# Optimization experiments

Measured on AMD Instinct MI355X. Metric: run time of the kernel, lower is better.

Reference implementation:

```python
import jax, jax.numpy as jnp
import numpy as np

B, S, D = 2, 2048, 1024
N_HEAD, D_ATTN = 16, 64


def setup_inputs() -> dict:
    key = jax.random.key(0)
    ks = jax.random.split(key, 5)
    x = jax.random.normal(ks[0], (B, S, D), dtype=jnp.float32)
    # causal mask: True = masked (as consumed by torch.masked_fill)
    mask = jnp.triu(jnp.ones((S, S), dtype=bool), k=1)
    scale = 0.02
    w_q = jax.random.normal(ks[1], (D, N_HEAD * D_ATTN), dtype=jnp.float32) * scale
    w_k = jax.random.normal(ks[2], (D, N_HEAD * D_ATTN), dtype=jnp.float32) * scale
    w_v = jax.random.normal(ks[3], (D, N_HEAD * D_ATTN), dtype=jnp.float32) * scale
    w_o = jax.random.normal(ks[4], (N_HEAD * D_ATTN, D), dtype=jnp.float32) * scale
    return {"x": x, "mask": mask, "w_q": w_q, "w_k": w_k, "w_v": w_v, "w_o": w_o}


def _split(t):
    # [B,S,H*Da] -> [B,H,S,Da]
    b, s, _ = t.shape
    return t.reshape(b, s, N_HEAD, D_ATTN).transpose(0, 2, 1, 3)


def reference(x, mask, w_q, w_k, w_v, w_o):
    q = _split(x @ w_q)
    k = _split(x @ w_k)
    v = _split(x @ w_v)
    scale = D_ATTN ** 0.5
    score = jnp.einsum("bhqd,bhkd->bhqk", q, k) / scale  # [B,H,S,S]
    score = jnp.where(mask, -jnp.inf, score)
    prob = jax.nn.softmax(score, axis=-1)
    out = jnp.einsum("bhqk,bhkd->bhqd", prob, v)
    out = out.transpose(0, 2, 1, 3).reshape(x.shape[0], x.shape[1], N_HEAD * D_ATTN)
    return out @ w_o
```

## Files before the change

kernel.cpp:

```cpp
#include <hip/hip_runtime.h>
#include <stdint.h>

using u16 = unsigned short;
using u32 = unsigned int;
using u64 = unsigned long long;

typedef float f32x4 __attribute__((ext_vector_type(4)));
typedef __bf16 bf16x8 __attribute__((ext_vector_type(8)));

#define DEV static __device__ __forceinline__

DEV u16 f2bf(float f) {
  u32 u = __float_as_uint(f);
  u += 0x7FFFu + ((u >> 16) & 1u);
  return (u16)(u >> 16);
}

DEV void gld16(const void* g, void* l) {
  __builtin_amdgcn_global_load_lds((__attribute__((address_space(1))) void*)g,
                                   (__attribute__((address_space(3))) void*)l,
                                   16, 0, 0);
}

__global__ void k_cvt_x(const float* __restrict__ x, u16* __restrict__ xb) {
  int i = (blockIdx.x * 256 + threadIdx.x) * 8;
  float4 a = *(const float4*)&x[i];
  float4 b = *(const float4*)&x[i + 4];
  __align__(16) u16 o[8];
  o[0] = f2bf(a.x); o[1] = f2bf(a.y); o[2] = f2bf(a.z); o[3] = f2bf(a.w);
  o[4] = f2bf(b.x); o[5] = f2bf(b.y); o[6] = f2bf(b.z); o[7] = f2bf(b.w);
  *(uint4*)&xb[i] = *(const uint4*)o;
}

__global__ void k_cvt_w(const float* __restrict__ w0, const float* __restrict__ w1,
                        const float* __restrict__ w2, const float* __restrict__ w3,
                        u16* __restrict__ t0, u16* __restrict__ t1,
                        u16* __restrict__ t2, u16* __restrict__ t3) {
  const float* w = blockIdx.z == 0 ? w0 : blockIdx.z == 1 ? w1 : blockIdx.z == 2 ? w2 : w3;
  u16* wt       = blockIdx.z == 0 ? t0 : blockIdx.z == 1 ? t1 : blockIdx.z == 2 ? t2 : t3;
  __shared__ __align__(16) float tile[64][68];
  const int tid = threadIdx.x;
  const int k0 = blockIdx.x * 64, n0 = blockIdx.y * 64;
#pragma unroll
  for (int i = 0; i < 4; ++i) {
    int c = tid + i * 256;
    int kr = c >> 4, col = (c & 15) * 4;
    *(float4*)&tile[kr][col] = *(const float4*)&w[(size_t)(k0 + kr) * 1024 + n0 + col];
  }
  __syncthreads();
#pragma unroll
  for (int i = 0; i < 2; ++i) {
    int c = tid + i * 256;
    int nr = c >> 3, kc = (c & 7) * 8;
    __align__(16) u16 o[8];
#pragma unroll
    for (int j = 0; j < 8; ++j) o[j] = f2bf(tile[kc + j][nr]);
    *(uint4*)&wt[(size_t)(n0 + nr) * 1024 + k0 + kc] = *(const uint4*)o;
  }
}

DEV void gemm_mainloop(const u16* __restrict__ A, const u16* __restrict__ Bt,
                       int m0, int n0, u16* Asb, u16* Bsb, f32x4 (&acc)[4][4]) {
  const int tid = threadIdx.x;
  const int lane = tid & 63;
  const int wv = tid >> 6;
  const int wm = (wv >> 1) * 64, wn = (wv & 1) * 64;

#pragma unroll
  for (int i = 0; i < 4; ++i)
#pragma unroll
    for (int j = 0; j < 4; ++j) {
      f32x4 z = {0.f, 0.f, 0.f, 0.f};
      acc[i][j] = z;
    }

  const int c0 = wv * 64 + lane, c1 = c0 + 256;
  const int r0 = c0 >> 2, r1 = c1 >> 2;
  const int b0 = (c0 & 3) ^ (r0 & 3) ^ ((r0 >> 2) & 3);
  const int b1 = (c1 & 3) ^ (r1 & 3) ^ ((r1 >> 2) & 3);
  const u16* ga0 = A + (size_t)(m0 + r0) * 1024 + b0 * 8;
  const u16* ga1 = A + (size_t)(m0 + r1) * 1024 + b1 * 8;
  const u16* gb0 = Bt + (size_t)(n0 + r0) * 1024 + b0 * 8;
  const u16* gb1 = Bt + (size_t)(n0 + r1) * 1024 + b1 * 8;
  u16* la0 = Asb + (wv * 64) * 8;
  u16* la1 = Asb + (wv * 64 + 256) * 8;
  u16* lb0 = Bsb + (wv * 64) * 8;
  u16* lb1 = Bsb + (wv * 64 + 256) * 8;

  int aoff[4], boff[4];
#pragma unroll
  for (int f = 0; f < 4; ++f) {
    int ra = wm + f * 16 + (lane & 15);
    aoff[f] = ra * 32 + (((lane >> 4) ^ (ra & 3) ^ ((ra >> 2) & 3)) * 8);
    int rb = wn + f * 16 + (lane & 15);
    boff[f] = rb * 32 + (((lane >> 4) ^ (rb & 3) ^ ((rb >> 2) & 3)) * 8);
  }

  for (int kt = 0; kt < 32; ++kt) {
    const int k0 = kt * 32;
    gld16(ga0 + k0, la0);
    gld16(ga1 + k0, la1);
    gld16(gb0 + k0, lb0);
    gld16(gb1 + k0, lb1);
    __syncthreads();
    bf16x8 af[4], bfv[4];
#pragma unroll
    for (int f = 0; f < 4; ++f) af[f] = *(const bf16x8*)&Asb[aoff[f]];
#pragma unroll
    for (int f = 0; f < 4; ++f) bfv[f] = *(const bf16x8*)&Bsb[boff[f]];
#pragma unroll
    for (int i = 0; i < 4; ++i)
#pragma unroll
      for (int j = 0; j < 4; ++j)
        acc[i][j] = __builtin_amdgcn_mfma_f32_16x16x32_bf16(af[i], bfv[j], acc[i][j], 0, 0, 0);
    __syncthreads();
  }
}

__global__ __launch_bounds__(256) void k_gemm_qkv(
    const u16* __restrict__ X, const u16* __restrict__ Wq, const u16* __restrict__ Wk,
    const u16* __restrict__ Wv, u16* __restrict__ Q, u16* __restrict__ K,
    u16* __restrict__ V) {
  __shared__ __align__(16) u16 Asb[128 * 32];
  __shared__ __align__(16) u16 Bsb[128 * 32];
  const int nb = blockIdx.x, mb = blockIdx.y;
  const int proj = nb >> 3, n0 = (nb & 7) * 128;
  const u16* W = proj == 0 ? Wq : proj == 1 ? Wk : Wv;
  u16* Dst = proj == 0 ? Q : proj == 1 ? K : V;
  const float scl = proj == 0 ? 0.125f * 1.4426950408889634f : 1.0f;
  f32x4 acc[4][4];
  gemm_mainloop(X, W, mb * 128, n0, Asb, Bsb, acc);
  const int lane = threadIdx.x & 63, wv = threadIdx.x >> 6;
  const int wm = (wv >> 1) * 64, wn = (wv & 1) * 64;
#pragma unroll
  for (int i = 0; i < 4; ++i)
#pragma unroll
    for (int j = 0; j < 4; ++j)
#pragma unroll
      for (int r = 0; r < 4; ++r) {
        int m = mb * 128 + wm + i * 16 + (lane >> 4) * 4 + r;
        int n = n0 + wn + j * 16 + (lane & 15);
        int b = m >> 11, s = m & 2047, h = n >> 6, d = n & 63;
        Dst[(size_t)((b * 16 + h) * 2048 + s) * 64 + d] = f2bf(acc[i][j][r] * scl);
      }
}

__global__ __launch_bounds__(256) void k_gemm_out(
    const u16* __restrict__ A, const u16* __restrict__ Wt, float* __restrict__ Out) {
  __shared__ __align__(16) u16 Asb[128 * 32];
  __shared__ __align__(16) u16 Bsb[128 * 32];
  const int nb = blockIdx.x, mb = blockIdx.y;
  f32x4 acc[4][4];
  gemm_mainloop(A, Wt, mb * 128, nb * 128, Asb, Bsb, acc);
  const int lane = threadIdx.x & 63, wv = threadIdx.x >> 6;
  const int wm = (wv >> 1) * 64, wn = (wv & 1) * 64;
#pragma unroll
  for (int i = 0; i < 4; ++i)
#pragma unroll
    for (int j = 0; j < 4; ++j)
#pragma unroll
      for (int r = 0; r < 4; ++r) {
        int m = mb * 128 + wm + i * 16 + (lane >> 4) * 4 + r;
        int n = nb * 128 + wn + j * 16 + (lane & 15);
        Out[(size_t)m * 1024 + n] = acc[i][j][r];
      }
}

__global__ void k_transpose_v(const u16* __restrict__ V, u16* __restrict__ Vt) {
  __shared__ __align__(16) u16 t[64][80];
  const int bh = blockIdx.y, s0 = blockIdx.x * 64;
  const int tid = threadIdx.x;
#pragma unroll
  for (int i = 0; i < 2; ++i) {
    int c = tid + i * 256;
    int sr = c >> 3, dc = (c & 7) * 8;
    *(uint4*)&t[sr][dc] = *(const uint4*)&V[((size_t)bh * 2048 + s0 + sr) * 64 + dc];
  }
  __syncthreads();
#pragma unroll
  for (int i = 0; i < 2; ++i) {
    int c = tid + i * 256;
    int dr = c >> 3, c7 = c & 7;
    __align__(8) u16 o[8];
#pragma unroll
    for (int j = 0; j < 8; ++j) o[j] = t[c7 * 8 + j][dr];
    int bp = ((c7 >> 1) & 1) * 32 + (c7 & 1) * 16 + ((c7 >> 2) & 1) * 4;
    u16* row = &Vt[((size_t)bh * 64 + dr) * 2048 + s0];
    *(u64*)&row[bp]     = *(const u64*)&o[0];
    *(u64*)&row[bp + 8] = *(const u64*)&o[4];
  }
}

__global__ __launch_bounds__(256) void k_attn(
    const u16* __restrict__ Qg, const u16* __restrict__ Kg,
    const u16* __restrict__ Vtg, u16* __restrict__ Og) {
  __shared__ __align__(16) u16 Ks[2][64 * 64];
  __shared__ __align__(16) u16 Vs[2][64 * 64];
  const int tid = threadIdx.x, lane = tid & 63, wv = tid >> 6;
  const int lo = lane & 15, hi = lane >> 4;
  const int jpair = blockIdx.x, bh = blockIdx.y;
  const u16* Qb = Qg + (size_t)bh * 2048 * 64;
  const u16* Kb = Kg + (size_t)bh * 2048 * 64;
  const u16* Vb = Vtg + (size_t)bh * 64 * 2048;
  const int b = bh >> 4, h = bh & 15;

  const int c0 = wv * 64 + lane, c1 = c0 + 256;
  const int r0 = c0 >> 3, r1 = c1 >> 3;
  const int e0 = ((c0 & 7) ^ (r0 & 7)) * 8;
  const int e1 = ((c1 & 7) ^ (r1 & 7)) * 8;

#pragma unroll 1
  for (int pass = 0; pass < 2; ++pass) {
    const int qt = pass == 0 ? jpair : 31 - jpair;
    const int q0 = qt * 64;
    const int nt = qt + 1;
    const int qq = q0 + wv * 16 + lo;

    bf16x8 qf[2];
#pragma unroll
    for (int kf = 0; kf < 2; ++kf)
      qf[kf] = *(const bf16x8*)&Qb[(size_t)(q0 + wv * 16 + lo) * 64 + kf * 32 + hi * 8];

    f32x4 ao[4];
#pragma unroll
    for (int df = 0; df < 4; ++df) {
      f32x4 z = {0.f, 0.f, 0.f, 0.f};
      ao[df] = z;
    }
    float m_run = -1e30f, l_run = 0.f;

    gld16(Kb + (size_t)r0 * 64 + e0, &Ks[0][wv * 512]);
    gld16(Kb + (size_t)r1 * 64 + e1, &Ks[0][wv * 512 + 2048]);
    gld16(Vb + (size_t)r0 * 2048 + e0, &Vs[0][wv * 512]);
    gld16(Vb + (size_t)r1 * 2048 + e1, &Vs[0][wv * 512 + 2048]);
    __syncthreads();

    int cur = 0;
#pragma unroll 1
    for (int t = 0; t < nt; ++t) {
      const int kv0 = t * 64;
      if (t + 1 < nt) {
        const int kn = kv0 + 64;
        gld16(Kb + (size_t)(kn + r0) * 64 + e0, &Ks[cur ^ 1][wv * 512]);
        gld16(Kb + (size_t)(kn + r1) * 64 + e1, &Ks[cur ^ 1][wv * 512 + 2048]);
        gld16(Vb + (size_t)r0 * 2048 + kn + e0, &Vs[cur ^ 1][wv * 512]);
        gld16(Vb + (size_t)r1 * 2048 + kn + e1, &Vs[cur ^ 1][wv * 512 + 2048]);
      }

      f32x4 sc[4];
#pragma unroll
      for (int cf = 0; cf < 4; ++cf) {
        f32x4 z = {0.f, 0.f, 0.f, 0.f};
        sc[cf] = z;
#pragma unroll
        for (int kf = 0; kf < 2; ++kf) {
          int row = cf * 16 + lo;
          int blk = ((kf * 4 + hi) ^ (row & 7)) * 8;
          bf16x8 kfr = *(const bf16x8*)&Ks[cur][row * 64 + blk];
          sc[cf] = __builtin_amdgcn_mfma_f32_16x16x32_bf16(kfr, qf[kf], sc[cf], 0, 0, 0);
        }
      }

      if (t == nt - 1) {
#pragma unroll
        for (int cf = 0; cf < 4; ++cf)
#pragma unroll
          for (int r = 0; r < 4; ++r) {
            int kk = kv0 + cf * 16 + hi * 4 + r;
            if (kk > qq) sc[cf][r] = -1e30f;
          }
      }

      float mx0 = fmaxf(fmaxf(sc[0][0], sc[0][1]), fmaxf(sc[0][2], sc[0][3]));
      float mx1 = fmaxf(fmaxf(sc[1][0], sc[1][1]), fmaxf(sc[1][2], sc[1][3]));
      float mx2 = fmaxf(fmaxf(sc[2][0], sc[2][1]), fmaxf(sc[2][2], sc[2][3]));
      float mx3 = fmaxf(fmaxf(sc[3][0], sc[3][1]), fmaxf(sc[3][2], sc[3][3]));
      float mx = fmaxf(fmaxf(mx0, mx1), fmaxf(mx2, mx3));
      mx = fmaxf(mx, __shfl_xor(mx, 16));
      mx = fmaxf(mx, __shfl_xor(mx, 32));

      if (__any(mx > m_run + 8.0f)) {
        float mnew = fmaxf(m_run, mx);
        float sclf = __builtin_amdgcn_exp2f(m_run - mnew);
        const int base = lane & 48;
#pragma unroll
        for (int r = 0; r < 4; ++r) {
          float s_r = __shfl(sclf, base + hi * 4 + r);
#pragma unroll
          for (int df = 0; df < 4; ++df) ao[df][r] *= s_r;
        }
        l_run *= sclf;
        m_run = mnew;
      }

      float pp[4];
      bf16x8 pa0, pa1;
#pragma unroll
      for (int cf = 0; cf < 4; ++cf) {
        float p0 = __builtin_amdgcn_exp2f(sc[cf][0] - m_run);
        float p1 = __builtin_amdgcn_exp2f(sc[cf][1] - m_run);
        float p2 = __builtin_amdgcn_exp2f(sc[cf][2] - m_run);
        float p3 = __builtin_amdgcn_exp2f(sc[cf][3] - m_run);
        pp[cf] = (p0 + p1) + (p2 + p3);
        bf16x8& pa = (cf & 1) ? pa1 : pa0;
        int j = (cf >> 1) * 4;
        pa[j] = (__bf16)p0; pa[j + 1] = (__bf16)p1;
        pa[j + 2] = (__bf16)p2; pa[j + 3] = (__bf16)p3;
      }
      float psum = (pp[0] + pp[1]) + (pp[2] + pp[3]);
      psum += __shfl_xor(psum, 16);
      psum += __shfl_xor(psum, 32);
      l_run += psum;

#pragma unroll
      for (int df = 0; df < 4; ++df) {
#pragma unroll
        for (int kf = 0; kf < 2; ++kf) {
          int row = df * 16 + lo;
          int blk = ((kf * 4 + hi) ^ (row & 7)) * 8;
          bf16x8 vfr = *(const bf16x8*)&Vs[cur][row * 64 + blk];
          ao[df] = __builtin_amdgcn_mfma_f32_16x16x32_bf16(kf == 0 ? pa0 : pa1, vfr,
                                                           ao[df], 0, 0, 0);
        }
      }
      __syncthreads();
      cur ^= 1;
    }

    float linv[4];
    const int base = lane & 48;
#pragma unroll
    for (int r = 0; r < 4; ++r) {
      float l_r = __shfl(l_run, base + hi * 4 + r);
      linv[r] = 1.0f / l_r;
    }
#pragma unroll
    for (int df = 0; df < 4; ++df)
#pragma unroll
      for (int r = 0; r < 4; ++r) {
        int s = q0 + wv * 16 + hi * 4 + r;
        int d = df * 16 + lo;
        Og[((size_t)(b * 2048 + s)) * 1024 + h * 64 + d] = f2bf(ao[df][r] * linv[r]);
      }
    __syncthreads();
  }
}

extern "C" void kernel_launch(void* const* d_in, const int* in_sizes, int n_in,
                              void* d_out, int out_size, void* d_ws, size_t ws_size,
                              hipStream_t stream) {
  const float* x = (const float*)d_in[0];
  const float* wq = (const float*)d_in[2];
  const float* wk = (const float*)d_in[3];
  const float* wv = (const float*)d_in[4];
  const float* wo = (const float*)d_in[5];

  char* ws = (char*)d_ws;
  u16* xb  = (u16*)(ws);
  u16* wqt = (u16*)(ws + 8388608);
  u16* wkt = (u16*)(ws + 8388608 + 2097152);
  u16* wvt = (u16*)(ws + 8388608 + 2 * 2097152);
  u16* wot = (u16*)(ws + 8388608 + 3 * 2097152);
  u16* qb  = (u16*)(ws + 16777216);
  u16* kb  = (u16*)(ws + 16777216 + 8388608);
  u16* vb  = (u16*)(ws + 16777216 + 2 * 8388608);
  u16* vt  = (u16*)(ws + 16777216 + 3 * 8388608);
  u16* ao  = (u16*)(ws + 16777216 + 4 * 8388608);

  k_cvt_x<<<dim3(2048), dim3(256), 0, stream>>>(x, xb);
  k_cvt_w<<<dim3(16, 16, 4), dim3(256), 0, stream>>>(wq, wk, wv, wo, wqt, wkt, wvt, wot);
  k_gemm_qkv<<<dim3(24, 32), dim3(256), 0, stream>>>(xb, wqt, wkt, wvt, qb, kb, vb);
  k_transpose_v<<<dim3(32, 32), dim3(256), 0, stream>>>(vb, vt);
  k_attn<<<dim3(16, 32), dim3(256), 0, stream>>>(qb, kb, vt, ao);
  k_gemm_out<<<dim3(8, 32), dim3(256), 0, stream>>>(ao, wot, (float*)d_out);
}
```

Measured before the change: 128.8 us.

## Double-buffer GEMM LDS tiles and fuse paired attention query tiles into one KV sweep

The GEMM mainloop now double-buffers its LDS tiles and prefetches the next K slice while computing the current one, which removes one barrier per iteration. The attention kernel processes both causal query tiles of a pair in a single sweep over K/V, so the shared prefix tiles are loaded once instead of twice. It also adds s_setprio around the MFMA sections and remaps blocks to XCDs so that the heads sharing K/V land together. The cost is doubled LDS in the GEMMs and higher register pressure from two sets of accumulators in attention.

```diff
diff --git a/kernel.cpp b/kernel.cpp
--- a/kernel.cpp
+++ b/kernel.cpp
@@ -82,10 +82,7 @@
   const u16* ga1 = A + (size_t)(m0 + r1) * 1024 + b1 * 8;
   const u16* gb0 = Bt + (size_t)(n0 + r0) * 1024 + b0 * 8;
   const u16* gb1 = Bt + (size_t)(n0 + r1) * 1024 + b1 * 8;
-  u16* la0 = Asb + (wv * 64) * 8;
-  u16* la1 = Asb + (wv * 64 + 256) * 8;
-  u16* lb0 = Bsb + (wv * 64) * 8;
-  u16* lb1 = Bsb + (wv * 64 + 256) * 8;
+  const int da0 = (wv * 64) * 8, da1 = (wv * 64 + 256) * 8;
 
   int aoff[4], boff[4];
 #pragma unroll
@@ -96,18 +93,27 @@
     boff[f] = rb * 32 + (((lane >> 4) ^ (rb & 3) ^ ((rb >> 2) & 3)) * 8);
   }
 
+  gld16(ga0, Asb + da0);
+  gld16(ga1, Asb + da1);
+  gld16(gb0, Bsb + da0);
+  gld16(gb1, Bsb + da1);
+  __syncthreads();
+
   for (int kt = 0; kt < 32; ++kt) {
-    const int k0 = kt * 32;
-    gld16(ga0 + k0, la0);
-    gld16(ga1 + k0, la1);
-    gld16(gb0 + k0, lb0);
-    gld16(gb1 + k0, lb1);
-    __syncthreads();
+    const int cur = (kt & 1) * 4096;
+    if (kt + 1 < 32) {
+      const int nxt = 4096 - cur;
+      const int k0 = (kt + 1) * 32;
+      gld16(ga0 + k0, Asb + nxt + da0);
+      gld16(ga1 + k0, Asb + nxt + da1);
+      gld16(gb0 + k0, Bsb + nxt + da0);
+      gld16(gb1 + k0, Bsb + nxt + da1);
+    }
     bf16x8 af[4], bfv[4];
 #pragma unroll
-    for (int f = 0; f < 4; ++f) af[f] = *(const bf16x8*)&Asb[aoff[f]];
-#pragma unroll
-    for (int f = 0; f < 4; ++f) bfv[f] = *(const bf16x8*)&Bsb[boff[f]];
+    for (int f = 0; f < 4; ++f) af[f] = *(const bf16x8*)&Asb[cur + aoff[f]];
+#pragma unroll
+    for (int f = 0; f < 4; ++f) bfv[f] = *(const bf16x8*)&Bsb[cur + boff[f]];
 #pragma unroll
     for (int i = 0; i < 4; ++i)
 #pragma unroll
@@ -121,8 +127,8 @@
     const u16* __restrict__ X, const u16* __restrict__ Wq, const u16* __restrict__ Wk,
     const u16* __restrict__ Wv, u16* __restrict__ Q, u16* __restrict__ K,
     u16* __restrict__ V) {
-  __shared__ __align__(16) u16 Asb[128 * 32];
-  __shared__ __align__(16) u16 Bsb[128 * 32];
+  __shared__ __align__(16) u16 Asb[2 * 128 * 32];
+  __shared__ __align__(16) u16 Bsb[2 * 128 * 32];
   const int nb = blockIdx.x, mb = blockIdx.y;
   const int proj = nb >> 3, n0 = (nb & 7) * 128;
   const u16* W = proj == 0 ? Wq : proj == 1 ? Wk : Wv;
@@ -147,8 +153,8 @@
 
 __global__ __launch_bounds__(256) void k_gemm_out(
     const u16* __restrict__ A, const u16* __restrict__ Wt, float* __restrict__ Out) {
-  __shared__ __align__(16) u16 Asb[128 * 32];
-  __shared__ __align__(16) u16 Bsb[128 * 32];
+  __shared__ __align__(16) u16 Asb[2 * 128 * 32];
+  __shared__ __align__(16) u16 Bsb[2 * 128 * 32];
   const int nb = blockIdx.x, mb = blockIdx.y;
   f32x4 acc[4][4];
   gemm_mainloop(A, Wt, mb * 128, nb * 128, Asb, Bsb, acc);
@@ -189,6 +195,79 @@
     *(u64*)&row[bp]     = *(const u64*)&o[0];
     *(u64*)&row[bp + 8] = *(const u64*)&o[4];
   }
+}
+
+DEV void qk_tile(const u16* Kc, const bf16x8 (&qf)[2], int lo, int hi, f32x4 (&sc)[4]) {
+#pragma unroll
+  for (int cf = 0; cf < 4; ++cf) {
+    f32x4 z = {0.f, 0.f, 0.f, 0.f};
+    sc[cf] = z;
+#pragma unroll
+    for (int kf = 0; kf < 2; ++kf) {
+      int row = cf * 16 + lo;
+      int blk = ((kf * 4 + hi) ^ (row & 7)) * 8;
+      bf16x8 kfr = *(const bf16x8*)&Kc[row * 64 + blk];
+      sc[cf] = __builtin_amdgcn_mfma_f32_16x16x32_bf16(kfr, qf[kf], sc[cf], 0, 0, 0);
+    }
+  }
+}
+
+DEV void sm_pv(f32x4 (&sc)[4], const u16* Vc, int lane, int lo, int hi,
+               float& m_run, float& l_run, f32x4 (&ao)[4]) {
+  float mx0 = fmaxf(fmaxf(sc[0][0], sc[0][1]), fmaxf(sc[0][2], sc[0][3]));
+  float mx1 = fmaxf(fmaxf(sc[1][0], sc[1][1]), fmaxf(sc[1][2], sc[1][3]));
+  float mx2 = fmaxf(fmaxf(sc[2][0], sc[2][1]), fmaxf(sc[2][2], sc[2][3]));
+  float mx3 = fmaxf(fmaxf(sc[3][0], sc[3][1]), fmaxf(sc[3][2], sc[3][3]));
+  float mx = fmaxf(fmaxf(mx0, mx1), fmaxf(mx2, mx3));
+  mx = fmaxf(mx, __shfl_xor(mx, 16));
+  mx = fmaxf(mx, __shfl_xor(mx, 32));
+
+  if (__any(mx > m_run + 8.0f)) {
+    float mnew = fmaxf(m_run, mx);
+    float sclf = __builtin_amdgcn_exp2f(m_run - mnew);
+    const int base = lane & 48;
+#pragma unroll
+    for (int r = 0; r < 4; ++r) {
+      float s_r = __shfl(sclf, base + hi * 4 + r);
+#pragma unroll
+      for (int df = 0; df < 4; ++df) ao[df][r] *= s_r;
+    }
+    l_run *= sclf;
+    m_run = mnew;
+  }
+
+  float pp[4];
+  bf16x8 pa0, pa1;
+#pragma unroll
+  for (int cf = 0; cf < 4; ++cf) {
+    float p0 = __builtin_amdgcn_exp2f(sc[cf][0] - m_run);
+    float p1 = __builtin_amdgcn_exp2f(sc[cf][1] - m_run);
+    float p2 = __builtin_amdgcn_exp2f(sc[cf][2] - m_run);
+    float p3 = __builtin_amdgcn_exp2f(sc[cf][3] - m_run);
+    pp[cf] = (p0 + p1) + (p2 + p3);
+    bf16x8& pa = (cf & 1) ? pa1 : pa0;
+    int j = (cf >> 1) * 4;
+    pa[j] = (__bf16)p0; pa[j + 1] = (__bf16)p1;
+    pa[j + 2] = (__bf16)p2; pa[j + 3] = (__bf16)p3;
+  }
+  float psum = (pp[0] + pp[1]) + (pp[2] + pp[3]);
+  psum += __shfl_xor(psum, 16);
+  psum += __shfl_xor(psum, 32);
+  l_run += psum;
+
+  __builtin_amdgcn_s_setprio(1);
+#pragma unroll
+  for (int df = 0; df < 4; ++df) {
+#pragma unroll
+    for (int kf = 0; kf < 2; ++kf) {
+      int row = df * 16 + lo;
+      int blk = ((kf * 4 + hi) ^ (row & 7)) * 8;
+      bf16x8 vfr = *(const bf16x8*)&Vc[row * 64 + blk];
+      ao[df] = __builtin_amdgcn_mfma_f32_16x16x32_bf16(kf == 0 ? pa0 : pa1, vfr,
+                                                       ao[df], 0, 0, 0);
+    }
+  }
+  __builtin_amdgcn_s_setprio(0);
 }
 
 __global__ __launch_bounds__(256) void k_attn(
@@ -198,137 +277,103 @@
   __shared__ __align__(16) u16 Vs[2][64 * 64];
   const int tid = threadIdx.x, lane = tid & 63, wv = tid >> 6;
   const int lo = lane & 15, hi = lane >> 4;
-  const int jpair = blockIdx.x, bh = blockIdx.y;
+
+  const int flat = blockIdx.y * 16 + blockIdx.x;
+  const int xcd = flat & 7, slot = flat >> 3;
+  const int bh = xcd * 4 + (slot >> 4);
+  const int jpair = slot & 15;
+
   const u16* Qb = Qg + (size_t)bh * 2048 * 64;
   const u16* Kb = Kg + (size_t)bh * 2048 * 64;
   const u16* Vb = Vtg + (size_t)bh * 64 * 2048;
   const int b = bh >> 4, h = bh & 15;
 
+  const int q0A = jpair * 64, q0B = (31 - jpair) * 64;
+  const int nta = jpair + 1, ntb = 32 - jpair;
+  const int qqA = q0A + wv * 16 + lo, qqB = q0B + wv * 16 + lo;
+
+  bf16x8 qfA[2], qfB[2];
+#pragma unroll
+  for (int kf = 0; kf < 2; ++kf) {
+    qfA[kf] = *(const bf16x8*)&Qb[(size_t)(q0A + wv * 16 + lo) * 64 + kf * 32 + hi * 8];
+    qfB[kf] = *(const bf16x8*)&Qb[(size_t)(q0B + wv * 16 + lo) * 64 + kf * 32 + hi * 8];
+  }
+
+  f32x4 aoA[4], aoB[4];
+#pragma unroll
+  for (int df = 0; df < 4; ++df) {
+    f32x4 z = {0.f, 0.f, 0.f, 0.f};
+    aoA[df] = z;
+    aoB[df] = z;
+  }
+  float mA = -1e30f, lA = 0.f, mB = -1e30f, lB = 0.f;
+
   const int c0 = wv * 64 + lane, c1 = c0 + 256;
   const int r0 = c0 >> 3, r1 = c1 >> 3;
   const int e0 = ((c0 & 7) ^ (r0 & 7)) * 8;
   const int e1 = ((c1 & 7) ^ (r1 & 7)) * 8;
 
+  gld16(Kb + (size_t)r0 * 64 + e0, &Ks[0][wv * 512]);
+  gld16(Kb + (size_t)r1 * 64 + e1, &Ks[0][wv * 512 + 2048]);
+  gld16(Vb + (size_t)r0 * 2048 + e0, &Vs[0][wv * 512]);
+  gld16(Vb + (size_t)r1 * 2048 + e1, &Vs[0][wv * 512 + 2048]);
+  __syncthreads();
+
 #pragma unroll 1
+  for (int t = 0; t < ntb; ++t) {
+    const u16* Kc = Ks[t & 1];
+    const u16* Vc = Vs[t & 1];
+    if (t + 1 < ntb) {
+      const int kn = (t + 1) * 64;
+      u16* kd = Ks[(t + 1) & 1];
+      u16* vd = Vs[(t + 1) & 1];
+      gld16(Kb + (size_t)(kn + r0) * 64 + e0, kd + wv * 512);
+      gld16(Kb + (size_t)(kn + r1) * 64 + e1, kd + wv * 512 + 2048);
+      gld16(Vb + (size_t)r0 * 2048 + kn + e0, vd + wv * 512);
+      gld16(Vb + (size_t)r1 * 2048 + kn + e1, vd + wv * 512 + 2048);
+    }
+    const bool doA = (t < nta);
+
+    f32x4 scB[4], scA[4];
+    __builtin_amdgcn_s_setprio(1);
+    qk_tile(Kc, qfB, lo, hi, scB);
+    if (doA) qk_tile(Kc, qfA, lo, hi, scA);
+    __builtin_amdgcn_s_setprio(0);
+
+    if (t == ntb - 1) {
+      const int kv0 = t * 64;
+#pragma unroll
+      for (int cf = 0; cf < 4; ++cf)
+#pragma unroll
+        for (int r = 0; r < 4; ++r) {
+          int kk = kv0 + cf * 16 + hi * 4 + r;
+          if (kk > qqB) scB[cf][r] = -1e30f;
+        }
+    }
+    if (doA && t == nta - 1) {
+      const int kv0 = t * 64;
+#pragma unroll
+      for (int cf = 0; cf < 4; ++cf)
+#pragma unroll
+        for (int r = 0; r < 4; ++r) {
+          int kk = kv0 + cf * 16 + hi * 4 + r;
+          if (kk > qqA) scA[cf][r] = -1e30f;
+        }
+    }
+
+    sm_pv(scB, Vc, lane, lo, hi, mB, lB, aoB);
+    if (doA) sm_pv(scA, Vc, lane, lo, hi, mA, lA, aoA);
+
+    __syncthreads();
+  }
+
+  const int base = lane & 48;
+#pragma unroll
   for (int pass = 0; pass < 2; ++pass) {
-    const int qt = pass == 0 ? jpair : 31 - jpair;
-    const int q0 = qt * 64;
-    const int nt = qt + 1;
-    const int qq = q0 + wv * 16 + lo;
-
-    bf16x8 qf[2];
-#pragma unroll
-    for (int kf = 0; kf < 2; ++kf)
-      qf[kf] = *(const bf16x8*)&Qb[(size_t)(q0 + wv * 16 + lo) * 64 + kf * 32 + hi * 8];
-
-    f32x4 ao[4];
-#pragma unroll
-    for (int df = 0; df < 4; ++df) {
-      f32x4 z = {0.f, 0.f, 0.f, 0.f};
-      ao[df] = z;
-    }
-    float m_run = -1e30f, l_run = 0.f;
-
-    gld16(Kb + (size_t)r0 * 64 + e0, &Ks[0][wv * 512]);
-    gld16(Kb + (size_t)r1 * 64 + e1, &Ks[0][wv * 512 + 2048]);
-    gld16(Vb + (size_t)r0 * 2048 + e0, &Vs[0][wv * 512]);
-    gld16(Vb + (size_t)r1 * 2048 + e1, &Vs[0][wv * 512 + 2048]);
-    __syncthreads();
-
-    int cur = 0;
-#pragma unroll 1
-    for (int t = 0; t < nt; ++t) {
-      const int kv0 = t * 64;
-      if (t + 1 < nt) {
-        const int kn = kv0 + 64;
-        gld16(Kb + (size_t)(kn + r0) * 64 + e0, &Ks[cur ^ 1][wv * 512]);
-        gld16(Kb + (size_t)(kn + r1) * 64 + e1, &Ks[cur ^ 1][wv * 512 + 2048]);
-        gld16(Vb + (size_t)r0 * 2048 + kn + e0, &Vs[cur ^ 1][wv * 512]);
-        gld16(Vb + (size_t)r1 * 2048 + kn + e1, &Vs[cur ^ 1][wv * 512 + 2048]);
-      }
-
-      f32x4 sc[4];
-#pragma unroll
-      for (int cf = 0; cf < 4; ++cf) {
-        f32x4 z = {0.f, 0.f, 0.f, 0.f};
-        sc[cf] = z;
-#pragma unroll
-        for (int kf = 0; kf < 2; ++kf) {
-          int row = cf * 16 + lo;
-          int blk = ((kf * 4 + hi) ^ (row & 7)) * 8;
-          bf16x8 kfr = *(const bf16x8*)&Ks[cur][row * 64 + blk];
-          sc[cf] = __builtin_amdgcn_mfma_f32_16x16x32_bf16(kfr, qf[kf], sc[cf], 0, 0, 0);
-        }
-      }
-
-      if (t == nt - 1) {
-#pragma unroll
-        for (int cf = 0; cf < 4; ++cf)
-#pragma unroll
-          for (int r = 0; r < 4; ++r) {
-            int kk = kv0 + cf * 16 + hi * 4 + r;
-            if (kk > qq) sc[cf][r] = -1e30f;
-          }
-      }
-
-      float mx0 = fmaxf(fmaxf(sc[0][0], sc[0][1]), fmaxf(sc[0][2], sc[0][3]));
-      float mx1 = fmaxf(fmaxf(sc[1][0], sc[1][1]), fmaxf(sc[1][2], sc[1][3]));
-      float mx2 = fmaxf(fmaxf(sc[2][0], sc[2][1]), fmaxf(sc[2][2], sc[2][3]));
-      float mx3 = fmaxf(fmaxf(sc[3][0], sc[3][1]), fmaxf(sc[3][2], sc[3][3]));
-      float mx = fmaxf(fmaxf(mx0, mx1), fmaxf(mx2, mx3));
-      mx = fmaxf(mx, __shfl_xor(mx, 16));
-      mx = fmaxf(mx, __shfl_xor(mx, 32));
-
-      if (__any(mx > m_run + 8.0f)) {
-        float mnew = fmaxf(m_run, mx);
-        float sclf = __builtin_amdgcn_exp2f(m_run - mnew);
-        const int base = lane & 48;
-#pragma unroll
-        for (int r = 0; r < 4; ++r) {
-          float s_r = __shfl(sclf, base + hi * 4 + r);
-#pragma unroll
-          for (int df = 0; df < 4; ++df) ao[df][r] *= s_r;
-        }
-        l_run *= sclf;
-        m_run = mnew;
-      }
-
-      float pp[4];
-      bf16x8 pa0, pa1;
-#pragma unroll
-      for (int cf = 0; cf < 4; ++cf) {
-        float p0 = __builtin_amdgcn_exp2f(sc[cf][0] - m_run);
-        float p1 = __builtin_amdgcn_exp2f(sc[cf][1] - m_run);
-        float p2 = __builtin_amdgcn_exp2f(sc[cf][2] - m_run);
-        float p3 = __builtin_amdgcn_exp2f(sc[cf][3] - m_run);
-        pp[cf] = (p0 + p1) + (p2 + p3);
-        bf16x8& pa = (cf & 1) ? pa1 : pa0;
-        int j = (cf >> 1) * 4;
-        pa[j] = (__bf16)p0; pa[j + 1] = (__bf16)p1;
-        pa[j + 2] = (__bf16)p2; pa[j + 3] = (__bf16)p3;
-      }
-      float psum = (pp[0] + pp[1]) + (pp[2] + pp[3]);
-      psum += __shfl_xor(psum, 16);
-      psum += __shfl_xor(psum, 32);
-      l_run += psum;
-
-#pragma unroll
-      for (int df = 0; df < 4; ++df) {
-#pragma unroll
-        for (int kf = 0; kf < 2; ++kf) {
-          int row = df * 16 + lo;
-          int blk = ((kf * 4 + hi) ^ (row & 7)) * 8;
-          bf16x8 vfr = *(const bf16x8*)&Vs[cur][row * 64 + blk];
-          ao[df] = __builtin_amdgcn_mfma_f32_16x16x32_bf16(kf == 0 ? pa0 : pa1, vfr,
-                                                           ao[df], 0, 0, 0);
-        }
-      }
-      __syncthreads();
-      cur ^= 1;
-    }
-
+    const f32x4* ao = pass == 0 ? aoA : aoB;
+    const float l_run = pass == 0 ? lA : lB;
+    const int q0 = pass == 0 ? q0A : q0B;
     float linv[4];
-    const int base = lane & 48;
 #pragma unroll
     for (int r = 0; r < 4; ++r) {
       float l_r = __shfl(l_run, base + hi * 4 + r);
@@ -342,7 +387,6 @@
         int d = df * 16 + lo;
         Og[((size_t)(b * 2048 + s)) * 1024 + h * 64 + d] = f2bf(ao[df][r] * linv[r]);
       }
-    __syncthreads();
   }
 }
 
```

After: 132.6 us. 2.9% more time.

## Fuse V transpose into QKV GEMM epilogue and remap attention grid per XCD

Applied to the files above, without the earlier changes.

The QKV GEMM now writes V directly in the transposed, permuted layout that attention consumes, which removes the separate transpose kernel and its round trip through global memory. The attention kernel drops the paired-pass scheme and launches one block per query tile, longest tiles first, with block indices remapped so the heads are grouped by XCD for L2 locality. MFMA phases are wrapped in s_setprio so matrix work gets scheduling priority. The risks are uncoalesced 8-byte scattered stores in the GEMM epilogue and load imbalance from one-tile blocks.

```diff
diff --git a/kernel.cpp b/kernel.cpp
--- a/kernel.cpp
+++ b/kernel.cpp
@@ -120,29 +120,49 @@
 __global__ __launch_bounds__(256) void k_gemm_qkv(
     const u16* __restrict__ X, const u16* __restrict__ Wq, const u16* __restrict__ Wk,
     const u16* __restrict__ Wv, u16* __restrict__ Q, u16* __restrict__ K,
-    u16* __restrict__ V) {
+    u16* __restrict__ Vt) {
   __shared__ __align__(16) u16 Asb[128 * 32];
   __shared__ __align__(16) u16 Bsb[128 * 32];
   const int nb = blockIdx.x, mb = blockIdx.y;
   const int proj = nb >> 3, n0 = (nb & 7) * 128;
   const u16* W = proj == 0 ? Wq : proj == 1 ? Wk : Wv;
-  u16* Dst = proj == 0 ? Q : proj == 1 ? K : V;
   const float scl = proj == 0 ? 0.125f * 1.4426950408889634f : 1.0f;
   f32x4 acc[4][4];
   gemm_mainloop(X, W, mb * 128, n0, Asb, Bsb, acc);
   const int lane = threadIdx.x & 63, wv = threadIdx.x >> 6;
+  const int lo = lane & 15, hi = lane >> 4;
   const int wm = (wv >> 1) * 64, wn = (wv & 1) * 64;
-#pragma unroll
-  for (int i = 0; i < 4; ++i)
-#pragma unroll
-    for (int j = 0; j < 4; ++j)
-#pragma unroll
-      for (int r = 0; r < 4; ++r) {
-        int m = mb * 128 + wm + i * 16 + (lane >> 4) * 4 + r;
-        int n = n0 + wn + j * 16 + (lane & 15);
-        int b = m >> 11, s = m & 2047, h = n >> 6, d = n & 63;
-        Dst[(size_t)((b * 16 + h) * 2048 + s) * 64 + d] = f2bf(acc[i][j][r] * scl);
+
+  if (proj == 2) {
+    const int stile = mb * 128 + wm;
+    const int b = stile >> 11, sb = stile & 2047;
+#pragma unroll
+    for (int i = 0; i < 4; ++i) {
+      const int kp = (i & 1) * 32 + (hi >> 1) * 16 + (hi & 1) * 8 + (i >> 1) * 4;
+#pragma unroll
+      for (int j = 0; j < 4; ++j) {
+        int n = n0 + wn + j * 16 + lo;
+        int h = n >> 6, d = n & 63;
+        __align__(8) u16 o[4];
+#pragma unroll
+        for (int r = 0; r < 4; ++r) o[r] = f2bf(acc[i][j][r]);
+        *(u64*)&Vt[((size_t)((b * 16 + h) * 64 + d)) * 2048 + sb + kp] = *(const u64*)o;
       }
+    }
+  } else {
+    u16* Dst = proj == 0 ? Q : K;
+#pragma unroll
+    for (int i = 0; i < 4; ++i)
+#pragma unroll
+      for (int j = 0; j < 4; ++j)
+#pragma unroll
+        for (int r = 0; r < 4; ++r) {
+          int m = mb * 128 + wm + i * 16 + hi * 4 + r;
+          int n = n0 + wn + j * 16 + lo;
+          int b = m >> 11, s = m & 2047, h = n >> 6, d = n & 63;
+          Dst[(size_t)((b * 16 + h) * 2048 + s) * 64 + d] = f2bf(acc[i][j][r] * scl);
+        }
+  }
 }
 
 __global__ __launch_bounds__(256) void k_gemm_out(
@@ -166,29 +186,77 @@
       }
 }
 
-__global__ void k_transpose_v(const u16* __restrict__ V, u16* __restrict__ Vt) {
-  __shared__ __align__(16) u16 t[64][80];
-  const int bh = blockIdx.y, s0 = blockIdx.x * 64;
-  const int tid = threadIdx.x;
-#pragma unroll
-  for (int i = 0; i < 2; ++i) {
-    int c = tid + i * 256;
-    int sr = c >> 3, dc = (c & 7) * 8;
-    *(uint4*)&t[sr][dc] = *(const uint4*)&V[((size_t)bh * 2048 + s0 + sr) * 64 + dc];
-  }
-  __syncthreads();
-#pragma unroll
-  for (int i = 0; i < 2; ++i) {
-    int c = tid + i * 256;
-    int dr = c >> 3, c7 = c & 7;
-    __align__(8) u16 o[8];
-#pragma unroll
-    for (int j = 0; j < 8; ++j) o[j] = t[c7 * 8 + j][dr];
-    int bp = ((c7 >> 1) & 1) * 32 + (c7 & 1) * 16 + ((c7 >> 2) & 1) * 4;
-    u16* row = &Vt[((size_t)bh * 64 + dr) * 2048 + s0];
-    *(u64*)&row[bp]     = *(const u64*)&o[0];
-    *(u64*)&row[bp + 8] = *(const u64*)&o[4];
-  }
+DEV void qk_tile(const u16* Kc, const bf16x8 (&qf)[2], int lo, int hi, f32x4 (&sc)[4]) {
+#pragma unroll
+  for (int cf = 0; cf < 4; ++cf) {
+    f32x4 z = {0.f, 0.f, 0.f, 0.f};
+    sc[cf] = z;
+#pragma unroll
+    for (int kf = 0; kf < 2; ++kf) {
+      int row = cf * 16 + lo;
+      int blk = ((kf * 4 + hi) ^ (row & 7)) * 8;
+      bf16x8 kfr = *(const bf16x8*)&Kc[row * 64 + blk];
+      sc[cf] = __builtin_amdgcn_mfma_f32_16x16x32_bf16(kfr, qf[kf], sc[cf], 0, 0, 0);
+    }
+  }
+}
+
+DEV void sm_pv(f32x4 (&sc)[4], const u16* Vc, int lane, int lo, int hi,
+               float& m_run, float& l_run, f32x4 (&ao)[4]) {
+  float mx0 = fmaxf(fmaxf(sc[0][0], sc[0][1]), fmaxf(sc[0][2], sc[0][3]));
+  float mx1 = fmaxf(fmaxf(sc[1][0], sc[1][1]), fmaxf(sc[1][2], sc[1][3]));
+  float mx2 = fmaxf(fmaxf(sc[2][0], sc[2][1]), fmaxf(sc[2][2], sc[2][3]));
+  float mx3 = fmaxf(fmaxf(sc[3][0], sc[3][1]), fmaxf(sc[3][2], sc[3][3]));
+  float mx = fmaxf(fmaxf(mx0, mx1), fmaxf(mx2, mx3));
+  mx = fmaxf(mx, __shfl_xor(mx, 16));
+  mx = fmaxf(mx, __shfl_xor(mx, 32));
+
+  if (__any(mx > m_run + 8.0f)) {
+    float mnew = fmaxf(m_run, mx);
+    float sclf = __builtin_amdgcn_exp2f(m_run - mnew);
+    const int base = lane & 48;
+#pragma unroll
+    for (int r = 0; r < 4; ++r) {
+      float s_r = __shfl(sclf, base + hi * 4 + r);
+#pragma unroll
+      for (int df = 0; df < 4; ++df) ao[df][r] *= s_r;
+    }
+    l_run *= sclf;
+    m_run = mnew;
+  }
+
+  float pp[4];
+  bf16x8 pa0, pa1;
+#pragma unroll
+  for (int cf = 0; cf < 4; ++cf) {
+    float p0 = __builtin_amdgcn_exp2f(sc[cf][0] - m_run);
+    float p1 = __builtin_amdgcn_exp2f(sc[cf][1] - m_run);
+    float p2 = __builtin_amdgcn_exp2f(sc[cf][2] - m_run);
+    float p3 = __builtin_amdgcn_exp2f(sc[cf][3] - m_run);
+    pp[cf] = (p0 + p1) + (p2 + p3);
+    bf16x8& pa = (cf & 1) ? pa1 : pa0;
+    int j = (cf >> 1) * 4;
+    pa[j] = (__bf16)p0; pa[j + 1] = (__bf16)p1;
+    pa[j + 2] = (__bf16)p2; pa[j + 3] = (__bf16)p3;
+  }
+  float psum = (pp[0] + pp[1]) + (pp[2] + pp[3]);
+  psum += __shfl_xor(psum, 16);
+  psum += __shfl_xor(psum, 32);
+  l_run += psum;
+
+  __builtin_amdgcn_s_setprio(1);
+#pragma unroll
+  for (int df = 0; df < 4; ++df) {
+#pragma unroll
+    for (int kf = 0; kf < 2; ++kf) {
+      int row = df * 16 + lo;
+      int blk = ((kf * 4 + hi) ^ (row & 7)) * 8;
+      bf16x8 vfr = *(const bf16x8*)&Vc[row * 64 + blk];
+      ao[df] = __builtin_amdgcn_mfma_f32_16x16x32_bf16(kf == 0 ? pa0 : pa1, vfr,
+                                                       ao[df], 0, 0, 0);
+    }
+  }
+  __builtin_amdgcn_s_setprio(0);
 }
 
 __global__ __launch_bounds__(256) void k_attn(
@@ -198,152 +266,95 @@
   __shared__ __align__(16) u16 Vs[2][64 * 64];
   const int tid = threadIdx.x, lane = tid & 63, wv = tid >> 6;
   const int lo = lane & 15, hi = lane >> 4;
-  const int jpair = blockIdx.x, bh = blockIdx.y;
+
+  const int flat = blockIdx.y * 32 + blockIdx.x;
+  const int xcd = flat & 7, slot = flat >> 3;
+  const int bh = xcd * 4 + (slot >> 5);
+  const int qt = 31 - (slot & 31);
+
   const u16* Qb = Qg + (size_t)bh * 2048 * 64;
   const u16* Kb = Kg + (size_t)bh * 2048 * 64;
   const u16* Vb = Vtg + (size_t)bh * 64 * 2048;
   const int b = bh >> 4, h = bh & 15;
 
+  const int q0 = qt * 64;
+  const int nt = qt + 1;
+  const int qq = q0 + wv * 16 + lo;
+
+  bf16x8 qf[2];
+#pragma unroll
+  for (int kf = 0; kf < 2; ++kf)
+    qf[kf] = *(const bf16x8*)&Qb[(size_t)(q0 + wv * 16 + lo) * 64 + kf * 32 + hi * 8];
+
+  f32x4 ao[4];
+#pragma unroll
+  for (int df = 0; df < 4; ++df) {
+    f32x4 z = {0.f, 0.f, 0.f, 0.f};
+    ao[df] = z;
+  }
+  float m_run = -1e30f, l_run = 0.f;
+
   const int c0 = wv * 64 + lane, c1 = c0 + 256;
   const int r0 = c0 >> 3, r1 = c1 >> 3;
   const int e0 = ((c0 & 7) ^ (r0 & 7)) * 8;
   const int e1 = ((c1 & 7) ^ (r1 & 7)) * 8;
 
+  gld16(Kb + (size_t)r0 * 64 + e0, &Ks[0][wv * 512]);
+  gld16(Kb + (size_t)r1 * 64 + e1, &Ks[0][wv * 512 + 2048]);
+  gld16(Vb + (size_t)r0 * 2048 + e0, &Vs[0][wv * 512]);
+  gld16(Vb + (size_t)r1 * 2048 + e1, &Vs[0][wv * 512 + 2048]);
+  __syncthreads();
+
 #pragma unroll 1
-  for (int pass = 0; pass < 2; ++pass) {
-    const int qt = pass == 0 ? jpair : 31 - jpair;
-    const int q0 = qt * 64;
-    const int nt = qt + 1;
-    const int qq = q0 + wv * 16 + lo;
-
-    bf16x8 qf[2];
-#pragma unroll
-    for (int kf = 0; kf < 2; ++kf)
-      qf[kf] = *(const bf16x8*)&Qb[(size_t)(q0 + wv * 16 + lo) * 64 + kf * 32 + hi * 8];
-
-    f32x4 ao[4];
-#pragma unroll
-    for (int df = 0; df < 4; ++df) {
-      f32x4 z = {0.f, 0.f, 0.f, 0.f};
-      ao[df] = z;
-    }
-    float m_run = -1e30f, l_run = 0.f;
-
-    gld16(Kb + (size_t)r0 * 64 + e0, &Ks[0][wv * 512]);
-    gld16(Kb + (size_t)r1 * 64 + e1, &Ks[0][wv * 512 + 2048]);
-    gld16(Vb + (size_t)r0 * 2048 + e0, &Vs[0][wv * 512]);
-    gld16(Vb + (size_t)r1 * 2048 + e1, &Vs[0][wv * 512 + 2048]);
+  for (int t = 0; t < nt; ++t) {
+    const u16* Kc = Ks[t & 1];
+    const u16* Vc = Vs[t & 1];
+    if (t + 1 < nt) {
+      const int kn = (t + 1) * 64;
+      u16* kd = Ks[(t + 1) & 1];
+      u16* vd = Vs[(t + 1) & 1];
+      gld16(Kb + (size_t)(kn + r0) * 64 + e0, kd + wv * 512);
+      gld16(Kb + (size_t)(kn + r1) * 64 + e1, kd + wv * 512 + 2048);
+      gld16(Vb + (size_t)r0 * 2048 + kn + e0, vd + wv * 512);
+      gld16(Vb + (size_t)r1 * 2048 + kn + e1, vd + wv * 512 + 2048);
+    }
+
+    f32x4 sc[4];
+    __builtin_amdgcn_s_setprio(1);
+    qk_tile(Kc, qf, lo, hi, sc);
+    __builtin_amdgcn_s_setprio(0);
+
+    if (t == nt - 1) {
+      const int kv0 = t * 64;
+#pragma unroll
+      for (int cf = 0; cf < 4; ++cf)
+#pragma unroll
+        for (int r = 0; r < 4; ++r) {
+          int kk = kv0 + cf * 16 + hi * 4 + r;
+          if (kk > qq) sc[cf][r] = -1e30f;
+        }
+    }
+
+    sm_pv(sc, Vc, lane, lo, hi, m_run, l_run, ao);
+
     __syncthreads();
-
-    int cur = 0;
-#pragma unroll 1
-    for (int t = 0; t < nt; ++t) {
-      const int kv0 = t * 64;
-      if (t + 1 < nt) {
-        const int kn = kv0 + 64;
-        gld16(Kb + (size_t)(kn + r0) * 64 + e0, &Ks[cur ^ 1][wv * 512]);
-        gld16(Kb + (size_t)(kn + r1) * 64 + e1, &Ks[cur ^ 1][wv * 512 + 2048]);
-        gld16(Vb + (size_t)r0 * 2048 + kn + e0, &Vs[cur ^ 1][wv * 512]);
-        gld16(Vb + (size_t)r1 * 2048 + kn + e1, &Vs[cur ^ 1][wv * 512 + 2048]);
-      }
-
-      f32x4 sc[4];
-#pragma unroll
-      for (int cf = 0; cf < 4; ++cf) {
-        f32x4 z = {0.f, 0.f, 0.f, 0.f};
-        sc[cf] = z;
-#pragma unroll
-        for (int kf = 0; kf < 2; ++kf) {
-          int row = cf * 16 + lo;
-          int blk = ((kf * 4 + hi) ^ (row & 7)) * 8;
-          bf16x8 kfr = *(const bf16x8*)&Ks[cur][row * 64 + blk];
-          sc[cf] = __builtin_amdgcn_mfma_f32_16x16x32_bf16(kfr, qf[kf], sc[cf], 0, 0, 0);
-        }
-      }
-
-      if (t == nt - 1) {
-#pragma unroll
-        for (int cf = 0; cf < 4; ++cf)
-#pragma unroll
-          for (int r = 0; r < 4; ++r) {
-            int kk = kv0 + cf * 16 + hi * 4 + r;
-            if (kk > qq) sc[cf][r] = -1e30f;
-          }
-      }
-
-      float mx0 = fmaxf(fmaxf(sc[0][0], sc[0][1]), fmaxf(sc[0][2], sc[0][3]));
-      float mx1 = fmaxf(fmaxf(sc[1][0], sc[1][1]), fmaxf(sc[1][2], sc[1][3]));
-      float mx2 = fmaxf(fmaxf(sc[2][0], sc[2][1]), fmaxf(sc[2][2], sc[2][3]));
-      float mx3 = fmaxf(fmaxf(sc[3][0], sc[3][1]), fmaxf(sc[3][2], sc[3][3]));
-      float mx = fmaxf(fmaxf(mx0, mx1), fmaxf(mx2, mx3));
-      mx = fmaxf(mx, __shfl_xor(mx, 16));
-      mx = fmaxf(mx, __shfl_xor(mx, 32));
-
-      if (__any(mx > m_run + 8.0f)) {
-        float mnew = fmaxf(m_run, mx);
-        float sclf = __builtin_amdgcn_exp2f(m_run - mnew);
-        const int base = lane & 48;
-#pragma unroll
-        for (int r = 0; r < 4; ++r) {
-          float s_r = __shfl(sclf, base + hi * 4 + r);
-#pragma unroll
-          for (int df = 0; df < 4; ++df) ao[df][r] *= s_r;
-        }
-        l_run *= sclf;
-        m_run = mnew;
-      }
-
-      float pp[4];
-      bf16x8 pa0, pa1;
-#pragma unroll
-      for (int cf = 0; cf < 4; ++cf) {
-        float p0 = __builtin_amdgcn_exp2f(sc[cf][0] - m_run);
-        float p1 = __builtin_amdgcn_exp2f(sc[cf][1] - m_run);
-        float p2 = __builtin_amdgcn_exp2f(sc[cf][2] - m_run);
-        float p3 = __builtin_amdgcn_exp2f(sc[cf][3] - m_run);
-        pp[cf] = (p0 + p1) + (p2 + p3);
-        bf16x8& pa = (cf & 1) ? pa1 : pa0;
-        int j = (cf >> 1) * 4;
-        pa[j] = (__bf16)p0; pa[j + 1] = (__bf16)p1;
-        pa[j + 2] = (__bf16)p2; pa[j + 3] = (__bf16)p3;
-      }
-      float psum = (pp[0] + pp[1]) + (pp[2] + pp[3]);
-      psum += __shfl_xor(psum, 16);
-      psum += __shfl_xor(psum, 32);
-      l_run += psum;
-
-#pragma unroll
-      for (int df = 0; df < 4; ++df) {
-#pragma unroll
-        for (int kf = 0; kf < 2; ++kf) {
-          int row = df * 16 + lo;
-          int blk = ((kf * 4 + hi) ^ (row & 7)) * 8;
-          bf16x8 vfr = *(const bf16x8*)&Vs[cur][row * 64 + blk];
-          ao[df] = __builtin_amdgcn_mfma_f32_16x16x32_bf16(kf == 0 ? pa0 : pa1, vfr,
-                                                           ao[df], 0, 0, 0);
-        }
-      }
-      __syncthreads();
-      cur ^= 1;
-    }
-
-    float linv[4];
-    const int base = lane & 48;
+  }
+
+  float linv[4];
+  const int base = lane & 48;
+#pragma unroll
+  for (int r = 0; r < 4; ++r) {
+    float l_r = __shfl(l_run, base + hi * 4 + r);
+    linv[r] = 1.0f / l_r;
+  }
+#pragma unroll
+  for (int df = 0; df < 4; ++df)
 #pragma unroll
     for (int r = 0; r < 4; ++r) {
-      float l_r = __shfl(l_run, base + hi * 4 + r);
-      linv[r] = 1.0f / l_r;
-    }
-#pragma unroll
-    for (int df = 0; df < 4; ++df)
-#pragma unroll
-      for (int r = 0; r < 4; ++r) {
-        int s = q0 + wv * 16 + hi * 4 + r;
-        int d = df * 16 + lo;
-        Og[((size_t)(b * 2048 + s)) * 1024 + h * 64 + d] = f2bf(ao[df][r] * linv[r]);
-      }
-    __syncthreads();
-  }
+      int s = q0 + wv * 16 + hi * 4 + r;
+      int d = df * 16 + lo;
+      Og[((size_t)(b * 2048 + s)) * 1024 + h * 64 + d] = f2bf(ao[df][r] * linv[r]);
+    }
 }
 
 extern "C" void kernel_launch(void* const* d_in, const int* in_sizes, int n_in,
@@ -363,14 +374,12 @@
   u16* wot = (u16*)(ws + 8388608 + 3 * 2097152);
   u16* qb  = (u16*)(ws + 16777216);
   u16* kb  = (u16*)(ws + 16777216 + 8388608);
-  u16* vb  = (u16*)(ws + 16777216 + 2 * 8388608);
   u16* vt  = (u16*)(ws + 16777216 + 3 * 8388608);
   u16* ao  = (u16*)(ws + 16777216 + 4 * 8388608);
 
   k_cvt_x<<<dim3(2048), dim3(256), 0, stream>>>(x, xb);
   k_cvt_w<<<dim3(16, 16, 4), dim3(256), 0, stream>>>(wq, wk, wv, wo, wqt, wkt, wvt, wot);
-  k_gemm_qkv<<<dim3(24, 32), dim3(256), 0, stream>>>(xb, wqt, wkt, wvt, qb, kb, vb);
-  k_transpose_v<<<dim3(32, 32), dim3(256), 0, stream>>>(vb, vt);
-  k_attn<<<dim3(16, 32), dim3(256), 0, stream>>>(qb, kb, vt, ao);
+  k_gemm_qkv<<<dim3(24, 32), dim3(256), 0, stream>>>(xb, wqt, wkt, wvt, qb, kb, vt);
+  k_attn<<<dim3(32, 32), dim3(256), 0, stream>>>(qb, kb, vt, ao);
   k_gemm_out<<<dim3(8, 32), dim3(256), 0, stream>>>(ao, wot, (float*)d_out);
 }
```

Result: slower. 146.1 us (+13.5%).
